# Performance work log

Hardware: AMD Instinct MI355X
Metric: run time of the kernel (lower is better)

The kernel has to match this reference:

```python
import jax, jax.numpy as jnp
import numpy as np
from jax.scipy.special import erf, erfc

N_ATOMS = 4096
BOX_L = 60.0
CUTOFF = 9.0
GRID = (64, 64, 64)
ORDER = 4
ALPHA = 0.34
COULOMB = 138.935456


def _bspline_weights(t, order):
    # Cardinal B-spline recursion (OpenMM/NNPOps convention).
    # w[..., j] = M_order(t + order - 1 - j), t in [0, 1)
    w = jnp.zeros(t.shape + (order,), t.dtype)
    w = w.at[..., 0].set(1.0 - t)
    w = w.at[..., 1].set(t)
    for k in range(3, order + 1):
        div = 1.0 / (k - 1)
        new = jnp.zeros_like(w)
        new = new.at[..., k - 1].set(div * t * w[..., k - 2])
        for j in range(1, k - 1):
            new = new.at[..., k - 1 - j].set(
                div * ((t + j) * w[..., k - 2 - j] + (k - j - t) * w[..., k - 1 - j]))
        new = new.at[..., 0].set(div * (1.0 - t) * w[..., 0])
        w = new
    return w


def _bspline_moduli(K, order):
    # |b(m)|^2 = 1 / |sum_k M_n(k+1) exp(2 pi i m k / K)|^2
    w = _bspline_weights(jnp.zeros((), jnp.float32), order)  # w[j] = M_n(n-1-j)
    mvals = w[::-1][1:]                                      # M_n(1), ..., M_n(n-1)
    data = jnp.zeros((K,), jnp.float32).at[jnp.arange(order - 1)].set(mvals)
    d2 = jnp.abs(jnp.fft.fft(data)) ** 2
    return 1.0 / jnp.maximum(d2, 1e-7)


def _min_image(delta, box, inv_box):
    s = delta @ inv_box
    s = s - jnp.round(s)
    return s @ box


def _pme_energy(positions, charges, box_vectors, exclusions):
    N = positions.shape[0]
    Kx, Ky, Kz = GRID
    inv_box = jnp.linalg.inv(box_vectors)

    # ---------------- direct space: erfc-screened pairwise sum with cutoff & exclusions
    delta = positions[:, None, :] - positions[None, :, :]          # [N,N,3]
    delta = _min_image(delta, box_vectors, inv_box)
    r2 = jnp.sum(delta * delta, axis=-1)                           # [N,N]
    rows = jnp.broadcast_to(jnp.arange(N)[:, None], exclusions.shape)
    excl_cols = jnp.where(exclusions >= 0, exclusions, rows)       # map padding -1 -> self
    excl_mask = jnp.zeros((N, N), bool).at[rows, excl_cols].set(True)
    pair_mask = jnp.triu(jnp.ones((N, N), bool), 1) & (r2 < CUTOFF ** 2) & (~excl_mask)
    r = jnp.sqrt(jnp.where(pair_mask, r2, 1.0))
    qq = charges[:, None] * charges[None, :]
    edir = COULOMB * jnp.sum(jnp.where(pair_mask, qq * erfc(ALPHA * r) / r, 0.0))

    # ---------------- reciprocal space: B-spline spread -> FFT -> influence function
    frac = positions @ inv_box
    frac = frac - jnp.floor(frac)                                  # wrap into [0,1)
    u = frac * jnp.asarray(GRID, frac.dtype)                       # [N,3] grid coords
    base = jnp.floor(u).astype(jnp.int32)
    t = u - jnp.floor(u)
    wx = _bspline_weights(t[:, 0], ORDER)                          # [N,order]
    wy = _bspline_weights(t[:, 1], ORDER)
    wz = _bspline_weights(t[:, 2], ORDER)
    offs = jnp.arange(ORDER, dtype=jnp.int32) - (ORDER - 1)        # weight j -> floor(u)-n+1+j
    ix = (base[:, 0:1] + offs) % Kx
    iy = (base[:, 1:2] + offs) % Ky
    iz = (base[:, 2:3] + offs) % Kz
    vals = (charges[:, None, None, None] * wx[:, :, None, None]
            * wy[:, None, :, None] * wz[:, None, None, :])         # [N,n,n,n]
    flat = (ix[:, :, None, None] * Ky + iy[:, None, :, None]) * Kz + iz[:, None, None, :]
    grid = jnp.zeros(Kx * Ky * Kz, positions.dtype).at[flat.reshape(-1)].add(
        vals.reshape(-1)).reshape(GRID)

    Fq = jnp.fft.fftn(grid)
    mx = (jnp.fft.fftfreq(Kx) * Kx).astype(positions.dtype)
    my = (jnp.fft.fftfreq(Ky) * Ky).astype(positions.dtype)
    mz = (jnp.fft.fftfreq(Kz) * Kz).astype(positions.dtype)
    m = jnp.stack(jnp.meshgrid(mx, my, mz, indexing='ij'), axis=-1)  # [Kx,Ky,Kz,3]
    kvec = m @ inv_box.T                                             # reciprocal vectors
    msq = jnp.sum(kvec * kvec, axis=-1)
    nonzero = msq > 0
    influence = jnp.where(nonzero,
                          jnp.exp(-(jnp.pi ** 2) * msq / ALPHA ** 2)
                          / jnp.where(nonzero, msq, 1.0), 0.0)
    bmod = (_bspline_moduli(Kx, ORDER)[:, None, None]
            * _bspline_moduli(Ky, ORDER)[None, :, None]
            * _bspline_moduli(Kz, ORDER)[None, None, :])
    V = jnp.abs(jnp.linalg.det(box_vectors))
    sq = Fq.real ** 2 + Fq.imag ** 2
    erec = COULOMB / (2.0 * jnp.pi * V) * jnp.sum(influence * bmod * sq)

    # self-energy correction
    eself = -COULOMB * ALPHA / jnp.sqrt(jnp.pi) * jnp.sum(charges ** 2)

    # exclusion correction: remove reciprocal contribution of excluded pairs
    de = positions[:, None, :] - positions[excl_cols]              # [N,E,3]
    de = _min_image(de, box_vectors, inv_box)
    re2 = jnp.sum(de * de, axis=-1)
    valid = (exclusions >= 0) & (re2 > 0)
    re = jnp.sqrt(jnp.where(valid, re2, 1.0))
    qe = charges[:, None] * charges[excl_cols]
    eexcl = -0.5 * COULOMB * jnp.sum(jnp.where(valid, qe * erf(ALPHA * re) / re, 0.0))

    return edir + erec + eself + eexcl


def setup_inputs():
    key = jax.random.key(0)
    k1, k2 = jax.random.split(key)
    positions = jax.random.uniform(k1, (N_ATOMS, 3), jnp.float32) * BOX_L
    charges = jax.random.normal(k2, (N_ATOMS,), jnp.float32) * 0.5
    charges = charges - jnp.mean(charges)  # neutral system
    box_vectors = jnp.eye(3, dtype=jnp.float32) * BOX_L
    idx = jnp.arange(N_ATOMS, dtype=jnp.int32)
    exclusions = jnp.stack([(idx - 1) % N_ATOMS, (idx + 1) % N_ATOMS], axis=1)  # symmetric chain
    return {"positions": positions, "charges": charges,
            "box_vectors": box_vectors, "exclusions": exclusions}


def reference(positions, charges, box_vectors, exclusions):
    return _pme_energy(positions, charges, box_vectors, exclusions)
```

## Files before the change

### kernel.cpp

```cpp
#include <hip/hip_runtime.h>
#include <math.h>
#include <stdint.h>

#define KG 64
#define KG3 (KG * KG * KG)
#define MZK 33
#define ALPHA 0.34f
#define COULOMB 138.935456f
#define CUTOFF2 81.0f
#define PI_F 3.14159265358979323846f

struct BoxInfo {
    float inv[9];
    float vol;
    bool diag;
};
__device__ __forceinline__ BoxInfo load_box(const float* __restrict__ box) {
    BoxInfo b;
    float b0 = box[0], b1 = box[1], b2 = box[2];
    float b3 = box[3], b4 = box[4], b5 = box[5];
    float b6 = box[6], b7 = box[7], b8 = box[8];
    float det = b0 * (b4 * b8 - b5 * b7) - b1 * (b3 * b8 - b5 * b6) + b2 * (b3 * b7 - b4 * b6);
    float id = 1.0f / det;
    b.inv[0] = (b4 * b8 - b5 * b7) * id;
    b.inv[1] = (b2 * b7 - b1 * b8) * id;
    b.inv[2] = (b1 * b5 - b2 * b4) * id;
    b.inv[3] = (b5 * b6 - b3 * b8) * id;
    b.inv[4] = (b0 * b8 - b2 * b6) * id;
    b.inv[5] = (b2 * b3 - b0 * b5) * id;
    b.inv[6] = (b3 * b7 - b4 * b6) * id;
    b.inv[7] = (b1 * b6 - b0 * b7) * id;
    b.inv[8] = (b0 * b4 - b1 * b3) * id;
    b.vol = fabsf(det);
    b.diag = (b1 == 0.0f) && (b2 == 0.0f) && (b3 == 0.0f) && (b5 == 0.0f) && (b6 == 0.0f) &&
             (b7 == 0.0f);
    return b;
}

__device__ __forceinline__ float erfc_fast(float x) {
    float t = __builtin_amdgcn_rcpf(fmaf(0.3275911f, x, 1.0f));
    float p = fmaf(t, 1.061405429f, -1.453152027f);
    p = fmaf(t, p, 1.421413741f);
    p = fmaf(t, p, -0.284496736f);
    p = fmaf(t, p, 0.254829592f);
    return t * p * __expf(-x * x);
}

__device__ __forceinline__ void bspline4(float t, float* w) {
    float w0 = 1.0f - t, w1 = t;
    float a2 = 0.5f * t * w1;
    float a1 = 0.5f * ((t + 1.0f) * w0 + (2.0f - t) * w1);
    float a0 = 0.5f * (1.0f - t) * w0;
    const float d = 1.0f / 3.0f;
    w[3] = d * t * a2;
    w[2] = d * ((t + 1.0f) * a1 + (3.0f - t) * a2);
    w[1] = d * ((t + 2.0f) * a0 + (2.0f - t) * a1);
    w[0] = d * (1.0f - t) * a0;
}

__global__ __launch_bounds__(256) void spread_kernel(const float* __restrict__ pos,
                                                     const float* __restrict__ chg,
                                                     const float* __restrict__ box,
                                                     float* __restrict__ grid,
                                                     float4* __restrict__ pxq, int N) {
    int t4 = blockIdx.x * blockDim.x + threadIdx.x;
    int i = t4 >> 2, jx = t4 & 3;
    if (i >= N) return;
    BoxInfo B = load_box(box);
    float p0 = pos[3 * i], p1 = pos[3 * i + 1], p2 = pos[3 * i + 2];
    float q = chg[i];
    if (jx == 0) pxq[i] = make_float4(p0, p1, p2, q);
    float w[3][4];
    int idx[3][4];
#pragma unroll
    for (int a = 0; a < 3; a++) {
        float f = p0 * B.inv[0 * 3 + a] + p1 * B.inv[1 * 3 + a] + p2 * B.inv[2 * 3 + a];
        f -= floorf(f);
        float u = f * (float)KG;
        float fu = floorf(u);
        int base = (int)fu;
        float tt = u - fu;
        bspline4(tt, w[a]);
#pragma unroll
        for (int j = 0; j < 4; j++) idx[a][j] = (base - 3 + j + 2 * KG) & (KG - 1);
    }
    float qx = q * w[0][jx];
    int bx = idx[0][jx] * KG;
#pragma unroll
    for (int jy = 0; jy < 4; jy++) {
        float qxy = qx * w[1][jy];
        int bxy = (bx + idx[1][jy]) * KG;
#pragma unroll
        for (int jz = 0; jz < 4; jz++) {
            atomicAdd(&grid[bxy + idx[2][jz]], qxy * w[2][jz]);
        }
    }
}

#define DIB 256
#define DJT 32
__global__ __launch_bounds__(256) void direct_kernel(const float4* __restrict__ pxq,
                                                     const float* __restrict__ box,
                                                     const int* __restrict__ excl, int N, int E,
                                                     double* __restrict__ partD) {
    int ib = blockIdx.x * DIB, jb = blockIdx.y * DJT;
    if (jb + DJT <= ib) return;

    __shared__ float4 sj[DJT];
    __shared__ double wsum[4];
    int tid = threadIdx.x;
    if (tid < DJT) {
        int jg0 = jb + tid;
        sj[tid] = (jg0 < N) ? pxq[jg0] : make_float4(0.0f, 0.0f, 0.0f, 0.0f);
    }
    __syncthreads();

    BoxInfo B = load_box(box);
    double e = 0.0;
    int i = ib + tid;
    if (i < N) {
        float4 me = pxq[i];
        float xi = me.x, yi = me.y, zi = me.z, qi = me.w;
        int ex0 = -1, ex1 = -1;
        int ne = (E < 8) ? E : 8;
        int ex[8];
        for (int k = 0; k < ne; k++) ex[k] = excl[i * E + k];

        float fsum = 0.0f;
        if (B.diag) {
            float Lx = box[0], Ly = box[4], Lz = box[8];
            float ivx = B.inv[0], ivy = B.inv[4], ivz = B.inv[8];
#pragma unroll 8
            for (int jj = 0; jj < DJT; jj++) {
                float4 o = sj[jj];
                int jg = jb + jj;
                float dx = xi - o.x, dy = yi - o.y, dz = zi - o.z;
                dx -= rintf(dx * ivx) * Lx;
                dy -= rintf(dy * ivy) * Ly;
                dz -= rintf(dz * ivz) * Lz;
                float r2 = fmaf(dx, dx, fmaf(dy, dy, dz * dz));
                bool valid = (r2 < CUTOFF2) & (jg > i) & (jg < N);
                for (int k = 0; k < ne; k++) valid = valid & (ex[k] != jg);
                float r2m = valid ? r2 : 1.0f;
                float rinv = __builtin_amdgcn_rsqf(r2m);
                float r = r2m * rinv;
                float g = erfc_fast(ALPHA * r) * rinv;
                float qqm = valid ? qi * o.w : 0.0f;
                fsum = fmaf(qqm, g, fsum);
            }
        } else {
#pragma unroll 4
            for (int jj = 0; jj < DJT; jj++) {
                float4 o = sj[jj];
                int jg = jb + jj;
                float dx = xi - o.x, dy = yi - o.y, dz = zi - o.z;
                float s0 = dx * B.inv[0] + dy * B.inv[3] + dz * B.inv[6];
                float s1 = dx * B.inv[1] + dy * B.inv[4] + dz * B.inv[7];
                float s2 = dx * B.inv[2] + dy * B.inv[5] + dz * B.inv[8];
                s0 -= rintf(s0);
                s1 -= rintf(s1);
                s2 -= rintf(s2);
                float ddx = s0 * box[0] + s1 * box[3] + s2 * box[6];
                float ddy = s0 * box[1] + s1 * box[4] + s2 * box[7];
                float ddz = s0 * box[2] + s1 * box[5] + s2 * box[8];
                float r2 = fmaf(ddx, ddx, fmaf(ddy, ddy, ddz * ddz));
                bool valid = (r2 < CUTOFF2) & (jg > i) & (jg < N);
                for (int k = 0; k < ne; k++) valid = valid & (ex[k] != jg);
                float r2m = valid ? r2 : 1.0f;
                float rinv = __builtin_amdgcn_rsqf(r2m);
                float r = r2m * rinv;
                float g = erfc_fast(ALPHA * r) * rinv;
                float qqm = valid ? qi * o.w : 0.0f;
                fsum = fmaf(qqm, g, fsum);
            }
        }
        e = (double)(COULOMB * fsum);

        if (jb == ib) {
            const float inv_sqrt_pi = 0.5641895835477563f;
            float corr = -ALPHA * inv_sqrt_pi * qi * qi;
            for (int k = 0; k < ne; k++) {
                int j = ex[k];
                if (j < 0) continue;
                float4 o = pxq[j];
                float dx = xi - o.x, dy = yi - o.y, dz = zi - o.z;
                if (B.diag) {
                    dx -= rintf(dx * B.inv[0]) * box[0];
                    dy -= rintf(dy * B.inv[4]) * box[4];
                    dz -= rintf(dz * B.inv[8]) * box[8];
                } else {
                    float s0 = dx * B.inv[0] + dy * B.inv[3] + dz * B.inv[6];
                    float s1 = dx * B.inv[1] + dy * B.inv[4] + dz * B.inv[7];
                    float s2 = dx * B.inv[2] + dy * B.inv[5] + dz * B.inv[8];
                    s0 -= rintf(s0);
                    s1 -= rintf(s1);
                    s2 -= rintf(s2);
                    dx = s0 * box[0] + s1 * box[3] + s2 * box[6];
                    dy = s0 * box[1] + s1 * box[4] + s2 * box[7];
                    dz = s0 * box[2] + s1 * box[5] + s2 * box[8];
                }
                float r2 = dx * dx + dy * dy + dz * dz;
                if (r2 > 0.0f) {
                    float rinv = __builtin_amdgcn_rsqf(r2);
                    float r = r2 * rinv;
                    float erfv = 1.0f - erfc_fast(ALPHA * r);
                    corr += -0.5f * qi * o.w * erfv * rinv;
                }
            }
            e += (double)(COULOMB * corr);
        }
    }
#pragma unroll
    for (int off = 32; off > 0; off >>= 1) e += __shfl_down(e, off, 64);
    if ((tid & 63) == 0) wsum[tid >> 6] = e;
    __syncthreads();
    if (tid == 0)
        partD[blockIdx.y * gridDim.x + blockIdx.x] = wsum[0] + wsum[1] + wsum[2] + wsum[3];
}

struct Tw8 {
    float wc[8], ws[8], c8, s8, c1, s1;
};
__device__ __forceinline__ Tw8 make_tw8(int m) {
    Tw8 T;
    float s1, c1;
    __sincosf(-2.0f * PI_F * (float)m / (float)KG, &s1, &c1);
    T.c1 = c1;
    T.s1 = s1;
    float c2 = c1 * c1 - s1 * s1, s2 = 2.0f * c1 * s1;
    float c4 = c2 * c2 - s2 * s2, s4 = 2.0f * c2 * s2;
    T.c8 = c4 * c4 - s4 * s4;
    T.s8 = 2.0f * c4 * s4;
    T.wc[0] = 1.0f;
    T.ws[0] = 0.0f;
    T.wc[1] = c1;
    T.ws[1] = s1;
    T.wc[2] = c2;
    T.ws[2] = s2;
    T.wc[3] = c2 * c1 - s2 * s1;
    T.ws[3] = c2 * s1 + s2 * c1;
    T.wc[4] = c4;
    T.ws[4] = s4;
    T.wc[5] = c4 * c1 - s4 * s1;
    T.ws[5] = c4 * s1 + s4 * c1;
    T.wc[6] = c4 * c2 - s4 * s2;
    T.ws[6] = c4 * s2 + s4 * c2;
    T.wc[7] = c4 * T.wc[3] - s4 * T.ws[3];
    T.ws[7] = c4 * T.ws[3] + s4 * T.wc[3];
    return T;
}

__global__ __launch_bounds__(256) void dft_z(const float* __restrict__ grid,
                                             float2* __restrict__ bufA) {
    __shared__ float g[4][KG];
    int tid = threadIdx.x, wv = tid >> 6, ln = tid & 63;
    int line = blockIdx.x * 4 + wv;
    g[wv][ln] = grid[line * KG + ln];
    __syncthreads();
    Tw8 T = make_tw8(ln);
    float rr[8] = {0}, ii[8] = {0};
#pragma unroll
    for (int s = 0; s < 8; s++) {
#pragma unroll
        for (int gg = 0; gg < 8; gg++) {
            float gv = g[wv][s * 8 + gg];
            rr[gg] = fmaf(gv, T.wc[gg], rr[gg]);
            ii[gg] = fmaf(gv, T.ws[gg], ii[gg]);
            float nc = T.wc[gg] * T.c8 - T.ws[gg] * T.s8;
            T.ws[gg] = T.wc[gg] * T.s8 + T.ws[gg] * T.c8;
            T.wc[gg] = nc;
        }
    }
    if (ln < MZK) {
        float re = ((rr[0] + rr[1]) + (rr[2] + rr[3])) + ((rr[4] + rr[5]) + (rr[6] + rr[7]));
        float im = ((ii[0] + ii[1]) + (ii[2] + ii[3])) + ((ii[4] + ii[5]) + (ii[6] + ii[7]));
        int ix = line >> 6, iy = line & 63;
        bufA[(ix * KG + ln) * KG + iy] = make_float2(re, im);
    }
}

__global__ __launch_bounds__(256) void dft_y(const float2* __restrict__ bufA,
                                             float2* __restrict__ bufB) {
    __shared__ float2 c[4][KG];
    int tid = threadIdx.x, wv = tid >> 6, ln = tid & 63;
    int idx = blockIdx.x * 4 + wv;
    if (idx >= KG * MZK) return;
    int ix = idx / MZK, mz = idx - ix * MZK;
    c[wv][ln] = bufA[(ix * KG + mz) * KG + ln];
    __syncthreads();
    Tw8 T = make_tw8(ln);
    float rr[8] = {0}, ii[8] = {0};
#pragma unroll
    for (int s = 0; s < 8; s++) {
#pragma unroll
        for (int gg = 0; gg < 8; gg++) {
            float2 a = c[wv][s * 8 + gg];
            rr[gg] += a.x * T.wc[gg] - a.y * T.ws[gg];
            ii[gg] += a.x * T.ws[gg] + a.y * T.wc[gg];
            float nc = T.wc[gg] * T.c8 - T.ws[gg] * T.s8;
            T.ws[gg] = T.wc[gg] * T.s8 + T.ws[gg] * T.c8;
            T.wc[gg] = nc;
        }
    }
    float re = ((rr[0] + rr[1]) + (rr[2] + rr[3])) + ((rr[4] + rr[5]) + (rr[6] + rr[7]));
    float im = ((ii[0] + ii[1]) + (ii[2] + ii[3])) + ((ii[4] + ii[5]) + (ii[6] + ii[7]));
    bufB[(ln * MZK + mz) * KG + ix] = make_float2(re, im);
}

__device__ __forceinline__ float bmod4(float c1, float s1) {
    float c2 = 2.0f * c1 * c1 - 1.0f;
    float s2 = 2.0f * s1 * c1;
    float br = (1.0f + 4.0f * c1 + c2) * (1.0f / 6.0f);
    float bi = (4.0f * s1 + s2) * (1.0f / 6.0f);
    float d2 = br * br + bi * bi;
    return 1.0f / fmaxf(d2, 1e-7f);
}

__global__ __launch_bounds__(256) void dft_x_reduce(const float2* __restrict__ bufB,
                                                    const float* __restrict__ box,
                                                    double* __restrict__ partR) {
    __shared__ float2 c[4][KG];
    int tid = threadIdx.x, wv = tid >> 6, ln = tid & 63;
    int idx = blockIdx.x * 4 + wv;
    if (idx >= KG * MZK) return;
    int my = idx / MZK, mz = idx - my * MZK;
    c[wv][ln] = bufB[(my * MZK + mz) * KG + ln];
    __syncthreads();
    Tw8 T = make_tw8(ln);
    float rr[8] = {0}, ii[8] = {0};
#pragma unroll
    for (int s = 0; s < 8; s++) {
#pragma unroll
        for (int gg = 0; gg < 8; gg++) {
            float2 a = c[wv][s * 8 + gg];
            rr[gg] += a.x * T.wc[gg] - a.y * T.ws[gg];
            ii[gg] += a.x * T.ws[gg] + a.y * T.wc[gg];
            float nc = T.wc[gg] * T.c8 - T.ws[gg] * T.s8;
            T.ws[gg] = T.wc[gg] * T.s8 + T.ws[gg] * T.c8;
            T.wc[gg] = nc;
        }
    }
    float re = ((rr[0] + rr[1]) + (rr[2] + rr[3])) + ((rr[4] + rr[5]) + (rr[6] + rr[7]));
    float im = ((ii[0] + ii[1]) + (ii[2] + ii[3])) + ((ii[4] + ii[5]) + (ii[6] + ii[7]));
    float sq = re * re + im * im;

    BoxInfo B = load_box(box);
    int mx = ln;
    int msx = (mx < KG / 2) ? mx : mx - KG;
    int msy = (my < KG / 2) ? my : my - KG;
    int msz = (mz < KG / 2) ? mz : mz - KG;
    float fmx = (float)msx, fmy = (float)msy, fmz = (float)msz;
    float kx = fmx * B.inv[0] + fmy * B.inv[1] + fmz * B.inv[2];
    float ky = fmx * B.inv[3] + fmy * B.inv[4] + fmz * B.inv[5];
    float kz = fmx * B.inv[6] + fmy * B.inv[7] + fmz * B.inv[8];
    float msq = kx * kx + ky * ky + kz * kz;
    const float cexp = (PI_F * PI_F) / (ALPHA * ALPHA);
    float infl = (msq > 0.0f) ? __expf(-cexp * msq) / msq : 0.0f;

    float bx_ = bmod4(T.c1, T.s1);
    float sy, cy, sz, cz;
    __sincosf(2.0f * PI_F * (float)my / (float)KG, &sy, &cy);
    __sincosf(2.0f * PI_F * (float)mz / (float)KG, &sz, &cz);
    float by_ = bmod4(cy, sy);
    float bz_ = bmod4(cz, sz);

    float wgt = (mz == 0 || mz == 32) ? 1.0f : 2.0f;
    float pref = COULOMB / (2.0f * PI_F * B.vol);
    double term = (double)(wgt * pref * infl * bx_ * by_ * bz_ * sq);

#pragma unroll
    for (int off = 32; off > 0; off >>= 1) term += __shfl_down(term, off, 64);
    if (ln == 0) partR[idx] = term;
}

__global__ __launch_bounds__(1024) void final_reduce(const double* __restrict__ parts, int n,
                                                     float* __restrict__ out) {
    __shared__ double wsum[16];
    int tid = threadIdx.x;
    double s = 0.0;
    for (int k = tid; k < n; k += 1024) s += parts[k];
#pragma unroll
    for (int off = 32; off > 0; off >>= 1) s += __shfl_down(s, off, 64);
    if ((tid & 63) == 0) wsum[tid >> 6] = s;
    __syncthreads();
    if (tid == 0) {
        double t = 0.0;
#pragma unroll
        for (int w = 0; w < 16; w++) t += wsum[w];
        out[0] = (float)t;
    }
}


extern "C" void kernel_launch(void* const* d_in, const int* in_sizes, int n_in,
                              void* d_out, int out_size, void* d_ws, size_t ws_size,
                              hipStream_t stream) {
    const float* pos = (const float*)d_in[0];
    const float* chg = (const float*)d_in[1];
    const float* box = (const float*)d_in[2];
    const int* excl = (const int*)d_in[3];
    int N = in_sizes[0] / 3;
    int E = in_sizes[3] / N;

    char* ws = (char*)d_ws;
    double* partD = (double*)(ws + 4096);
    double* partR = (double*)(ws + 20480);
    double* parts = (double*)(ws + 4096);
    float* grid = (float*)(ws + 65536);
    float2* bufA = (float2*)(ws + 65536 + 4 * (size_t)KG3);
    float2* bufB = (float2*)(ws + 65536 + 12 * (size_t)KG3);
    float4* pxq = (float4*)bufB;

    hipMemsetAsync(ws, 0, 65536 + 4 * (size_t)KG3, stream);

    spread_kernel<<<(4 * N + 255) / 256, 256, 0, stream>>>(pos, chg, box, grid, pxq, N);

    int nib = (N + DIB - 1) / DIB;
    int njt = (N + DJT - 1) / DJT;
    dim3 dg(nib, njt);
    direct_kernel<<<dg, 256, 0, stream>>>(pxq, box, excl, N, E, partD);

    dft_z<<<KG * KG / 4, 256, 0, stream>>>(grid, bufA);
    int nlines = KG * MZK;
    dft_y<<<(nlines + 3) / 4, 256, 0, stream>>>(bufA, bufB);
    dft_x_reduce<<<(nlines + 3) / 4, 256, 0, stream>>>(bufB, box, partR);

    int nparts = nib * njt + nlines;
    final_reduce<<<1, 1024, 0, stream>>>(parts, nparts, (float*)d_out);
}
```

Before: 132.5 us.

## Fuse spread with direct sum, merge z/y DFTs, fold final reduce into x-DFT

Charge spreading and the direct-space pair sum now run as different block ranges of one launch. The z and y DFT passes are merged into one 512-thread kernel per x-plane that keeps the intermediate in shared memory. The final reduction moves into the x-DFT kernel through a last-block atomic counter. Together these drop the launch count from six to three and remove the bufA round trip through global memory. The cost is that the y pass runs on only 64 blocks, giving low parallelism, and every direct block now reads positions from the strided pos and chg arrays instead of packed float4s.

```diff
diff --git a/kernel.cpp b/kernel.cpp
--- a/kernel.cpp
+++ b/kernel.cpp
@@ -9,6 +9,8 @@
 #define COULOMB 138.935456f
 #define CUTOFF2 81.0f
 #define PI_F 3.14159265358979323846f
+#define DIB 256
+#define DJT 32
 
 struct BoxInfo {
     float inv[9];
@@ -56,166 +58,6 @@
     w[2] = d * ((t + 1.0f) * a1 + (3.0f - t) * a2);
     w[1] = d * ((t + 2.0f) * a0 + (2.0f - t) * a1);
     w[0] = d * (1.0f - t) * a0;
-}
-
-__global__ __launch_bounds__(256) void spread_kernel(const float* __restrict__ pos,
-                                                     const float* __restrict__ chg,
-                                                     const float* __restrict__ box,
-                                                     float* __restrict__ grid,
-                                                     float4* __restrict__ pxq, int N) {
-    int t4 = blockIdx.x * blockDim.x + threadIdx.x;
-    int i = t4 >> 2, jx = t4 & 3;
-    if (i >= N) return;
-    BoxInfo B = load_box(box);
-    float p0 = pos[3 * i], p1 = pos[3 * i + 1], p2 = pos[3 * i + 2];
-    float q = chg[i];
-    if (jx == 0) pxq[i] = make_float4(p0, p1, p2, q);
-    float w[3][4];
-    int idx[3][4];
-#pragma unroll
-    for (int a = 0; a < 3; a++) {
-        float f = p0 * B.inv[0 * 3 + a] + p1 * B.inv[1 * 3 + a] + p2 * B.inv[2 * 3 + a];
-        f -= floorf(f);
-        float u = f * (float)KG;
-        float fu = floorf(u);
-        int base = (int)fu;
-        float tt = u - fu;
-        bspline4(tt, w[a]);
-#pragma unroll
-        for (int j = 0; j < 4; j++) idx[a][j] = (base - 3 + j + 2 * KG) & (KG - 1);
-    }
-    float qx = q * w[0][jx];
-    int bx = idx[0][jx] * KG;
-#pragma unroll
-    for (int jy = 0; jy < 4; jy++) {
-        float qxy = qx * w[1][jy];
-        int bxy = (bx + idx[1][jy]) * KG;
-#pragma unroll
-        for (int jz = 0; jz < 4; jz++) {
-            atomicAdd(&grid[bxy + idx[2][jz]], qxy * w[2][jz]);
-        }
-    }
-}
-
-#define DIB 256
-#define DJT 32
-__global__ __launch_bounds__(256) void direct_kernel(const float4* __restrict__ pxq,
-                                                     const float* __restrict__ box,
-                                                     const int* __restrict__ excl, int N, int E,
-                                                     double* __restrict__ partD) {
-    int ib = blockIdx.x * DIB, jb = blockIdx.y * DJT;
-    if (jb + DJT <= ib) return;
-
-    __shared__ float4 sj[DJT];
-    __shared__ double wsum[4];
-    int tid = threadIdx.x;
-    if (tid < DJT) {
-        int jg0 = jb + tid;
-        sj[tid] = (jg0 < N) ? pxq[jg0] : make_float4(0.0f, 0.0f, 0.0f, 0.0f);
-    }
-    __syncthreads();
-
-    BoxInfo B = load_box(box);
-    double e = 0.0;
-    int i = ib + tid;
-    if (i < N) {
-        float4 me = pxq[i];
-        float xi = me.x, yi = me.y, zi = me.z, qi = me.w;
-        int ex0 = -1, ex1 = -1;
-        int ne = (E < 8) ? E : 8;
-        int ex[8];
-        for (int k = 0; k < ne; k++) ex[k] = excl[i * E + k];
-
-        float fsum = 0.0f;
-        if (B.diag) {
-            float Lx = box[0], Ly = box[4], Lz = box[8];
-            float ivx = B.inv[0], ivy = B.inv[4], ivz = B.inv[8];
-#pragma unroll 8
-            for (int jj = 0; jj < DJT; jj++) {
-                float4 o = sj[jj];
-                int jg = jb + jj;
-                float dx = xi - o.x, dy = yi - o.y, dz = zi - o.z;
-                dx -= rintf(dx * ivx) * Lx;
-                dy -= rintf(dy * ivy) * Ly;
-                dz -= rintf(dz * ivz) * Lz;
-                float r2 = fmaf(dx, dx, fmaf(dy, dy, dz * dz));
-                bool valid = (r2 < CUTOFF2) & (jg > i) & (jg < N);
-                for (int k = 0; k < ne; k++) valid = valid & (ex[k] != jg);
-                float r2m = valid ? r2 : 1.0f;
-                float rinv = __builtin_amdgcn_rsqf(r2m);
-                float r = r2m * rinv;
-                float g = erfc_fast(ALPHA * r) * rinv;
-                float qqm = valid ? qi * o.w : 0.0f;
-                fsum = fmaf(qqm, g, fsum);
-            }
-        } else {
-#pragma unroll 4
-            for (int jj = 0; jj < DJT; jj++) {
-                float4 o = sj[jj];
-                int jg = jb + jj;
-                float dx = xi - o.x, dy = yi - o.y, dz = zi - o.z;
-                float s0 = dx * B.inv[0] + dy * B.inv[3] + dz * B.inv[6];
-                float s1 = dx * B.inv[1] + dy * B.inv[4] + dz * B.inv[7];
-                float s2 = dx * B.inv[2] + dy * B.inv[5] + dz * B.inv[8];
-                s0 -= rintf(s0);
-                s1 -= rintf(s1);
-                s2 -= rintf(s2);
-                float ddx = s0 * box[0] + s1 * box[3] + s2 * box[6];
-                float ddy = s0 * box[1] + s1 * box[4] + s2 * box[7];
-                float ddz = s0 * box[2] + s1 * box[5] + s2 * box[8];
-                float r2 = fmaf(ddx, ddx, fmaf(ddy, ddy, ddz * ddz));
-                bool valid = (r2 < CUTOFF2) & (jg > i) & (jg < N);
-                for (int k = 0; k < ne; k++) valid = valid & (ex[k] != jg);
-                float r2m = valid ? r2 : 1.0f;
-                float rinv = __builtin_amdgcn_rsqf(r2m);
-                float r = r2m * rinv;
-                float g = erfc_fast(ALPHA * r) * rinv;
-                float qqm = valid ? qi * o.w : 0.0f;
-                fsum = fmaf(qqm, g, fsum);
-            }
-        }
-        e = (double)(COULOMB * fsum);
-
-        if (jb == ib) {
-            const float inv_sqrt_pi = 0.5641895835477563f;
-            float corr = -ALPHA * inv_sqrt_pi * qi * qi;
-            for (int k = 0; k < ne; k++) {
-                int j = ex[k];
-                if (j < 0) continue;
-                float4 o = pxq[j];
-                float dx = xi - o.x, dy = yi - o.y, dz = zi - o.z;
-                if (B.diag) {
-                    dx -= rintf(dx * B.inv[0]) * box[0];
-                    dy -= rintf(dy * B.inv[4]) * box[4];
-                    dz -= rintf(dz * B.inv[8]) * box[8];
-                } else {
-                    float s0 = dx * B.inv[0] + dy * B.inv[3] + dz * B.inv[6];
-                    float s1 = dx * B.inv[1] + dy * B.inv[4] + dz * B.inv[7];
-                    float s2 = dx * B.inv[2] + dy * B.inv[5] + dz * B.inv[8];
-                    s0 -= rintf(s0);
-                    s1 -= rintf(s1);
-                    s2 -= rintf(s2);
-                    dx = s0 * box[0] + s1 * box[3] + s2 * box[6];
-                    dy = s0 * box[1] + s1 * box[4] + s2 * box[7];
-                    dz = s0 * box[2] + s1 * box[5] + s2 * box[8];
-                }
-                float r2 = dx * dx + dy * dy + dz * dz;
-                if (r2 > 0.0f) {
-                    float rinv = __builtin_amdgcn_rsqf(r2);
-                    float r = r2 * rinv;
-                    float erfv = 1.0f - erfc_fast(ALPHA * r);
-                    corr += -0.5f * qi * o.w * erfv * rinv;
-                }
-            }
-            e += (double)(COULOMB * corr);
-        }
-    }
-#pragma unroll
-    for (int off = 32; off > 0; off >>= 1) e += __shfl_down(e, off, 64);
-    if ((tid & 63) == 0) wsum[tid >> 6] = e;
-    __syncthreads();
-    if (tid == 0)
-        partD[blockIdx.y * gridDim.x + blockIdx.x] = wsum[0] + wsum[1] + wsum[2] + wsum[3];
 }
 
 struct Tw8 {
@@ -250,63 +92,6 @@
     return T;
 }
 
-__global__ __launch_bounds__(256) void dft_z(const float* __restrict__ grid,
-                                             float2* __restrict__ bufA) {
-    __shared__ float g[4][KG];
-    int tid = threadIdx.x, wv = tid >> 6, ln = tid & 63;
-    int line = blockIdx.x * 4 + wv;
-    g[wv][ln] = grid[line * KG + ln];
-    __syncthreads();
-    Tw8 T = make_tw8(ln);
-    float rr[8] = {0}, ii[8] = {0};
-#pragma unroll
-    for (int s = 0; s < 8; s++) {
-#pragma unroll
-        for (int gg = 0; gg < 8; gg++) {
-            float gv = g[wv][s * 8 + gg];
-            rr[gg] = fmaf(gv, T.wc[gg], rr[gg]);
-            ii[gg] = fmaf(gv, T.ws[gg], ii[gg]);
-            float nc = T.wc[gg] * T.c8 - T.ws[gg] * T.s8;
-            T.ws[gg] = T.wc[gg] * T.s8 + T.ws[gg] * T.c8;
-            T.wc[gg] = nc;
-        }
-    }
-    if (ln < MZK) {
-        float re = ((rr[0] + rr[1]) + (rr[2] + rr[3])) + ((rr[4] + rr[5]) + (rr[6] + rr[7]));
-        float im = ((ii[0] + ii[1]) + (ii[2] + ii[3])) + ((ii[4] + ii[5]) + (ii[6] + ii[7]));
-        int ix = line >> 6, iy = line & 63;
-        bufA[(ix * KG + ln) * KG + iy] = make_float2(re, im);
-    }
-}
-
-__global__ __launch_bounds__(256) void dft_y(const float2* __restrict__ bufA,
-                                             float2* __restrict__ bufB) {
-    __shared__ float2 c[4][KG];
-    int tid = threadIdx.x, wv = tid >> 6, ln = tid & 63;
-    int idx = blockIdx.x * 4 + wv;
-    if (idx >= KG * MZK) return;
-    int ix = idx / MZK, mz = idx - ix * MZK;
-    c[wv][ln] = bufA[(ix * KG + mz) * KG + ln];
-    __syncthreads();
-    Tw8 T = make_tw8(ln);
-    float rr[8] = {0}, ii[8] = {0};
-#pragma unroll
-    for (int s = 0; s < 8; s++) {
-#pragma unroll
-        for (int gg = 0; gg < 8; gg++) {
-            float2 a = c[wv][s * 8 + gg];
-            rr[gg] += a.x * T.wc[gg] - a.y * T.ws[gg];
-            ii[gg] += a.x * T.ws[gg] + a.y * T.wc[gg];
-            float nc = T.wc[gg] * T.c8 - T.ws[gg] * T.s8;
-            T.ws[gg] = T.wc[gg] * T.s8 + T.ws[gg] * T.c8;
-            T.wc[gg] = nc;
-        }
-    }
-    float re = ((rr[0] + rr[1]) + (rr[2] + rr[3])) + ((rr[4] + rr[5]) + (rr[6] + rr[7]));
-    float im = ((ii[0] + ii[1]) + (ii[2] + ii[3])) + ((ii[4] + ii[5]) + (ii[6] + ii[7]));
-    bufB[(ln * MZK + mz) * KG + ix] = make_float2(re, im);
-}
-
 __device__ __forceinline__ float bmod4(float c1, float s1) {
     float c2 = 2.0f * c1 * c1 - 1.0f;
     float s2 = 2.0f * s1 * c1;
@@ -316,28 +101,272 @@
     return 1.0f / fmaxf(d2, 1e-7f);
 }
 
-__global__ __launch_bounds__(256) void dft_x_reduce(const float2* __restrict__ bufB,
-                                                    const float* __restrict__ box,
-                                                    double* __restrict__ partR) {
+__global__ __launch_bounds__(256) void spread_direct(const float* __restrict__ pos,
+                                                     const float* __restrict__ chg,
+                                                     const float* __restrict__ box,
+                                                     const int* __restrict__ excl, int N, int E,
+                                                     float* __restrict__ grid,
+                                                     double* __restrict__ partD) {
+    int tid = threadIdx.x;
+    const int nib = (N + DIB - 1) / DIB;
+    const int njt = (N + DJT - 1) / DJT;
+    const int DU = nib * njt;
+    int u = blockIdx.x;
+
+    if (u >= DU) {
+        int t4 = (u - DU) * 256 + tid;
+        int i = t4 >> 2, jx = t4 & 3;
+        if (i >= N) return;
+        BoxInfo B = load_box(box);
+        float p0 = pos[3 * i], p1 = pos[3 * i + 1], p2 = pos[3 * i + 2];
+        float q = chg[i];
+        float w[3][4];
+        int idx[3][4];
+#pragma unroll
+        for (int a = 0; a < 3; a++) {
+            float f = p0 * B.inv[0 * 3 + a] + p1 * B.inv[1 * 3 + a] + p2 * B.inv[2 * 3 + a];
+            f -= floorf(f);
+            float uu = f * (float)KG;
+            float fu = floorf(uu);
+            int base = (int)fu;
+            float tt = uu - fu;
+            bspline4(tt, w[a]);
+#pragma unroll
+            for (int j = 0; j < 4; j++) idx[a][j] = (base - 3 + j + 2 * KG) & (KG - 1);
+        }
+        float qx = q * w[0][jx];
+        int bx = idx[0][jx] * KG;
+#pragma unroll
+        for (int jy = 0; jy < 4; jy++) {
+            float qxy = qx * w[1][jy];
+            int bxy = (bx + idx[1][jy]) * KG;
+#pragma unroll
+            for (int jz = 0; jz < 4; jz++) {
+                atomicAdd(&grid[bxy + idx[2][jz]], qxy * w[2][jz]);
+            }
+        }
+        return;
+    }
+
+    int du = u;
+    int ib = (du % nib) * DIB, jb = (du / nib) * DJT;
+    if (jb + DJT <= ib) {
+        if (tid == 0) partD[du] = 0.0;
+        return;
+    }
+
+    __shared__ float4 sj[DJT];
+    __shared__ double wsum[4];
+    if (tid < DJT) {
+        int jg0 = jb + tid;
+        sj[tid] = (jg0 < N) ? make_float4(pos[3 * jg0], pos[3 * jg0 + 1], pos[3 * jg0 + 2],
+                                          chg[jg0])
+                            : make_float4(0.0f, 0.0f, 0.0f, 0.0f);
+    }
+    __syncthreads();
+
+    BoxInfo B = load_box(box);
+    double e = 0.0;
+    int i = ib + tid;
+    if (i < N) {
+        float xi = pos[3 * i], yi = pos[3 * i + 1], zi = pos[3 * i + 2], qi = chg[i];
+        int ne = (E < 8) ? E : 8;
+        int ex[8];
+        for (int k = 0; k < ne; k++) ex[k] = excl[i * E + k];
+
+        float fsum = 0.0f;
+        if (B.diag) {
+            float Lx = box[0], Ly = box[4], Lz = box[8];
+            float ivx = B.inv[0], ivy = B.inv[4], ivz = B.inv[8];
+#pragma unroll 8
+            for (int jj = 0; jj < DJT; jj++) {
+                float4 o = sj[jj];
+                int jg = jb + jj;
+                float dx = xi - o.x, dy = yi - o.y, dz = zi - o.z;
+                dx -= rintf(dx * ivx) * Lx;
+                dy -= rintf(dy * ivy) * Ly;
+                dz -= rintf(dz * ivz) * Lz;
+                float r2 = fmaf(dx, dx, fmaf(dy, dy, dz * dz));
+                bool valid = (r2 < CUTOFF2) & (jg > i) & (jg < N);
+                for (int k = 0; k < ne; k++) valid = valid & (ex[k] != jg);
+                float r2m = valid ? r2 : 1.0f;
+                float rinv = __builtin_amdgcn_rsqf(r2m);
+                float r = r2m * rinv;
+                float g = erfc_fast(ALPHA * r) * rinv;
+                float qqm = valid ? qi * o.w : 0.0f;
+                fsum = fmaf(qqm, g, fsum);
+            }
+        } else {
+#pragma unroll 4
+            for (int jj = 0; jj < DJT; jj++) {
+                float4 o = sj[jj];
+                int jg = jb + jj;
+                float dx = xi - o.x, dy = yi - o.y, dz = zi - o.z;
+                float s0 = dx * B.inv[0] + dy * B.inv[3] + dz * B.inv[6];
+                float s1 = dx * B.inv[1] + dy * B.inv[4] + dz * B.inv[7];
+                float s2 = dx * B.inv[2] + dy * B.inv[5] + dz * B.inv[8];
+                s0 -= rintf(s0);
+                s1 -= rintf(s1);
+                s2 -= rintf(s2);
+                float ddx = s0 * box[0] + s1 * box[3] + s2 * box[6];
+                float ddy = s0 * box[1] + s1 * box[4] + s2 * box[7];
+                float ddz = s0 * box[2] + s1 * box[5] + s2 * box[8];
+                float r2 = fmaf(ddx, ddx, fmaf(ddy, ddy, ddz * ddz));
+                bool valid = (r2 < CUTOFF2) & (jg > i) & (jg < N);
+                for (int k = 0; k < ne; k++) valid = valid & (ex[k] != jg);
+                float r2m = valid ? r2 : 1.0f;
+                float rinv = __builtin_amdgcn_rsqf(r2m);
+                float r = r2m * rinv;
+                float g = erfc_fast(ALPHA * r) * rinv;
+                float qqm = valid ? qi * o.w : 0.0f;
+                fsum = fmaf(qqm, g, fsum);
+            }
+        }
+        e = (double)(COULOMB * fsum);
+
+        if (jb == ib) {
+            const float inv_sqrt_pi = 0.5641895835477563f;
+            float corr = -ALPHA * inv_sqrt_pi * qi * qi;
+            for (int k = 0; k < ne; k++) {
+                int j = ex[k];
+                if (j < 0) continue;
+                float ox = pos[3 * j], oy = pos[3 * j + 1], oz = pos[3 * j + 2];
+                float qj = chg[j];
+                float dx = xi - ox, dy = yi - oy, dz = zi - oz;
+                if (B.diag) {
+                    dx -= rintf(dx * B.inv[0]) * box[0];
+                    dy -= rintf(dy * B.inv[4]) * box[4];
+                    dz -= rintf(dz * B.inv[8]) * box[8];
+                } else {
+                    float s0 = dx * B.inv[0] + dy * B.inv[3] + dz * B.inv[6];
+                    float s1 = dx * B.inv[1] + dy * B.inv[4] + dz * B.inv[7];
+                    float s2 = dx * B.inv[2] + dy * B.inv[5] + dz * B.inv[8];
+                    s0 -= rintf(s0);
+                    s1 -= rintf(s1);
+                    s2 -= rintf(s2);
+                    dx = s0 * box[0] + s1 * box[3] + s2 * box[6];
+                    dy = s0 * box[1] + s1 * box[4] + s2 * box[7];
+                    dz = s0 * box[2] + s1 * box[5] + s2 * box[8];
+                }
+                float r2 = dx * dx + dy * dy + dz * dz;
+                if (r2 > 0.0f) {
+                    float rinv = __builtin_amdgcn_rsqf(r2);
+                    float r = r2 * rinv;
+                    float erfv = 1.0f - erfc_fast(ALPHA * r);
+                    corr += -0.5f * qi * qj * erfv * rinv;
+                }
+            }
+            e += (double)(COULOMB * corr);
+        }
+    }
+#pragma unroll
+    for (int off = 32; off > 0; off >>= 1) e += __shfl_down(e, off, 64);
+    if ((tid & 63) == 0) wsum[tid >> 6] = e;
+    __syncthreads();
+    if (tid == 0) partD[du] = wsum[0] + wsum[1] + wsum[2] + wsum[3];
+}
+
+__global__ __launch_bounds__(512) void dft_zy(const float* __restrict__ grid,
+                                              float2* __restrict__ bufB) {
+    __shared__ float gin[KG * KG];
+    __shared__ float zre[KG * MZK];
+    __shared__ float zim[KG * MZK];
+    int tid = threadIdx.x, wv = tid >> 6, ln = tid & 63;
+    int ix = blockIdx.x;
+
+    const float4* g4 = reinterpret_cast<const float4*>(grid + ix * (KG * KG));
+    float4* s4 = reinterpret_cast<float4*>(gin);
+#pragma unroll
+    for (int k = 0; k < 2; k++) s4[k * 512 + tid] = g4[k * 512 + tid];
+    __syncthreads();
+
+    Tw8 T0 = make_tw8(ln);
+
+#pragma unroll
+    for (int it = 0; it < 8; it++) {
+        int iy = wv * 8 + it;
+        float wc[8], ws_[8];
+#pragma unroll
+        for (int g = 0; g < 8; g++) {
+            wc[g] = T0.wc[g];
+            ws_[g] = T0.ws[g];
+        }
+        float rr[8] = {0, 0, 0, 0, 0, 0, 0, 0}, ii[8] = {0, 0, 0, 0, 0, 0, 0, 0};
+#pragma unroll
+        for (int s = 0; s < 8; s++) {
+#pragma unroll
+            for (int g = 0; g < 8; g++) {
+                float gv = gin[iy * KG + s * 8 + g];
+                rr[g] = fmaf(gv, wc[g], rr[g]);
+                ii[g] = fmaf(gv, ws_[g], ii[g]);
+                float nc = wc[g] * T0.c8 - ws_[g] * T0.s8;
+                ws_[g] = wc[g] * T0.s8 + ws_[g] * T0.c8;
+                wc[g] = nc;
+            }
+        }
+        if (ln < MZK) {
+            float re = ((rr[0] + rr[1]) + (rr[2] + rr[3])) + ((rr[4] + rr[5]) + (rr[6] + rr[7]));
+            float im = ((ii[0] + ii[1]) + (ii[2] + ii[3])) + ((ii[4] + ii[5]) + (ii[6] + ii[7]));
+            zre[iy * MZK + ln] = re;
+            zim[iy * MZK + ln] = im;
+        }
+    }
+    __syncthreads();
+
+    for (int mz = wv; mz < MZK; mz += 8) {
+        float wc[8], ws_[8];
+#pragma unroll
+        for (int g = 0; g < 8; g++) {
+            wc[g] = T0.wc[g];
+            ws_[g] = T0.ws[g];
+        }
+        float rr[8] = {0, 0, 0, 0, 0, 0, 0, 0}, ii[8] = {0, 0, 0, 0, 0, 0, 0, 0};
+#pragma unroll
+        for (int s = 0; s < 8; s++) {
+#pragma unroll
+            for (int g = 0; g < 8; g++) {
+                int iy = s * 8 + g;
+                float ar = zre[iy * MZK + mz];
+                float ai = zim[iy * MZK + mz];
+                rr[g] += ar * wc[g] - ai * ws_[g];
+                ii[g] += ar * ws_[g] + ai * wc[g];
+                float nc = wc[g] * T0.c8 - ws_[g] * T0.s8;
+                ws_[g] = wc[g] * T0.s8 + ws_[g] * T0.c8;
+                wc[g] = nc;
+            }
+        }
+        float re = ((rr[0] + rr[1]) + (rr[2] + rr[3])) + ((rr[4] + rr[5]) + (rr[6] + rr[7]));
+        float im = ((ii[0] + ii[1]) + (ii[2] + ii[3])) + ((ii[4] + ii[5]) + (ii[6] + ii[7]));
+        bufB[(ln * MZK + mz) * KG + ix] = make_float2(re, im);
+    }
+}
+
+__global__ __launch_bounds__(256) void dft_x_final(const float2* __restrict__ bufB,
+                                                   const float* __restrict__ box,
+                                                   double* __restrict__ partR,
+                                                   const double* __restrict__ parts, int np,
+                                                   unsigned* __restrict__ cnt,
+                                                   float* __restrict__ out) {
     __shared__ float2 c[4][KG];
+    __shared__ double fw[4];
+    __shared__ unsigned lastFlag;
     int tid = threadIdx.x, wv = tid >> 6, ln = tid & 63;
     int idx = blockIdx.x * 4 + wv;
-    if (idx >= KG * MZK) return;
     int my = idx / MZK, mz = idx - my * MZK;
     c[wv][ln] = bufB[(my * MZK + mz) * KG + ln];
     __syncthreads();
     Tw8 T = make_tw8(ln);
-    float rr[8] = {0}, ii[8] = {0};
+    float rr[8] = {0, 0, 0, 0, 0, 0, 0, 0}, ii[8] = {0, 0, 0, 0, 0, 0, 0, 0};
 #pragma unroll
     for (int s = 0; s < 8; s++) {
 #pragma unroll
-        for (int gg = 0; gg < 8; gg++) {
-            float2 a = c[wv][s * 8 + gg];
-            rr[gg] += a.x * T.wc[gg] - a.y * T.ws[gg];
-            ii[gg] += a.x * T.ws[gg] + a.y * T.wc[gg];
-            float nc = T.wc[gg] * T.c8 - T.ws[gg] * T.s8;
-            T.ws[gg] = T.wc[gg] * T.s8 + T.ws[gg] * T.c8;
-            T.wc[gg] = nc;
+        for (int g = 0; g < 8; g++) {
+            float2 a = c[wv][s * 8 + g];
+            rr[g] += a.x * T.wc[g] - a.y * T.ws[g];
+            ii[g] += a.x * T.ws[g] + a.y * T.wc[g];
+            float nc = T.wc[g] * T.c8 - T.ws[g] * T.s8;
+            T.ws[g] = T.wc[g] * T.s8 + T.ws[g] * T.c8;
+            T.wc[g] = nc;
         }
     }
     float re = ((rr[0] + rr[1]) + (rr[2] + rr[3])) + ((rr[4] + rr[5]) + (rr[6] + rr[7]));
@@ -371,23 +400,24 @@
 #pragma unroll
     for (int off = 32; off > 0; off >>= 1) term += __shfl_down(term, off, 64);
     if (ln == 0) partR[idx] = term;
-}
-
-__global__ __launch_bounds__(1024) void final_reduce(const double* __restrict__ parts, int n,
-                                                     float* __restrict__ out) {
-    __shared__ double wsum[16];
-    int tid = threadIdx.x;
-    double s = 0.0;
-    for (int k = tid; k < n; k += 1024) s += parts[k];
-#pragma unroll
-    for (int off = 32; off > 0; off >>= 1) s += __shfl_down(s, off, 64);
-    if ((tid & 63) == 0) wsum[tid >> 6] = s;
+
     __syncthreads();
     if (tid == 0) {
-        double t = 0.0;
-#pragma unroll
-        for (int w = 0; w < 16; w++) t += wsum[w];
-        out[0] = (float)t;
+        __threadfence();
+        unsigned old = atomicAdd(cnt, 1u);
+        lastFlag = (old == gridDim.x - 1) ? 1u : 0u;
+    }
+    __syncthreads();
+    if (lastFlag) {
+        if (tid == 0) __threadfence();
+        __syncthreads();
+        double s = 0.0;
+        for (int k = tid; k < np; k += 256) s += parts[k];
+#pragma unroll
+        for (int off = 32; off > 0; off >>= 1) s += __shfl_down(s, off, 64);
+        if ((tid & 63) == 0) fw[tid >> 6] = s;
+        __syncthreads();
+        if (tid == 0) out[0] = (float)(fw[0] + fw[1] + fw[2] + fw[3]);
     }
 }
 
@@ -403,28 +433,25 @@
     int E = in_sizes[3] / N;
 
     char* ws = (char*)d_ws;
+    unsigned* cnt = (unsigned*)ws;
     double* partD = (double*)(ws + 4096);
     double* partR = (double*)(ws + 20480);
-    double* parts = (double*)(ws + 4096);
     float* grid = (float*)(ws + 65536);
-    float2* bufA = (float2*)(ws + 65536 + 4 * (size_t)KG3);
-    float2* bufB = (float2*)(ws + 65536 + 12 * (size_t)KG3);
-    float4* pxq = (float4*)bufB;
+    float2* bufB = (float2*)(ws + 65536 + 4 * (size_t)KG3);
+    float* outp = (float*)d_out;
+
+    const int nib = (N + DIB - 1) / DIB;
+    const int njt = (N + DJT - 1) / DJT;
+    const int DU = nib * njt;
+    const int SB = (4 * N + 255) / 256;
+    const int nlines = KG * MZK;
+    const int np = DU + nlines;
 
     hipMemsetAsync(ws, 0, 65536 + 4 * (size_t)KG3, stream);
 
-    spread_kernel<<<(4 * N + 255) / 256, 256, 0, stream>>>(pos, chg, box, grid, pxq, N);
-
-    int nib = (N + DIB - 1) / DIB;
-    int njt = (N + DJT - 1) / DJT;
-    dim3 dg(nib, njt);
-    direct_kernel<<<dg, 256, 0, stream>>>(pxq, box, excl, N, E, partD);
-
-    dft_z<<<KG * KG / 4, 256, 0, stream>>>(grid, bufA);
-    int nlines = KG * MZK;
-    dft_y<<<(nlines + 3) / 4, 256, 0, stream>>>(bufA, bufB);
-    dft_x_reduce<<<(nlines + 3) / 4, 256, 0, stream>>>(bufB, box, partR);
-
-    int nparts = nib * njt + nlines;
-    final_reduce<<<1, 1024, 0, stream>>>(parts, nparts, (float*)d_out);
-}
+    spread_direct<<<DU + SB, 256, 0, stream>>>(pos, chg, box, excl, N, E, grid, partD);
+
+    dft_zy<<<KG, 512, 0, stream>>>(grid, bufB);
+
+    dft_x_final<<<nlines / 4, 256, 0, stream>>>(bufB, box, partR, partD, np, cnt, outp);
+}
```

Measured after the change: 210.5 us. +58.9%, slower.

## Fuse spread with direct sum and fold final reduction into last DFT kernel

Applied to the files above, without the earlier changes.

Merges the charge-spreading and direct-space kernels into one launch, with block ranges partitioned between the two tasks. The direct part now reads positions and charges straight from the inputs instead of a packed float4 buffer. The final reduction moves into the x-DFT kernel using an atomic counter that picks the last block to finish. Two kernel launches and their serial dependencies go away, at the cost of strided uncoalesced position loads, a fence plus atomic per block, and a serialized tail reduction in the last block.

```diff
diff --git a/kernel.cpp b/kernel.cpp
--- a/kernel.cpp
+++ b/kernel.cpp
@@ -9,6 +9,8 @@
 #define COULOMB 138.935456f
 #define CUTOFF2 81.0f
 #define PI_F 3.14159265358979323846f
+#define DIB 256
+#define DJT 32
 
 struct BoxInfo {
     float inv[9];
@@ -58,60 +60,108 @@
     w[0] = d * (1.0f - t) * a0;
 }
 
-__global__ __launch_bounds__(256) void spread_kernel(const float* __restrict__ pos,
+struct Tw8 {
+    float wc[8], ws[8], c8, s8, c1, s1;
+};
+__device__ __forceinline__ Tw8 make_tw8(int m) {
+    Tw8 T;
+    float s1, c1;
+    __sincosf(-2.0f * PI_F * (float)m / (float)KG, &s1, &c1);
+    T.c1 = c1;
+    T.s1 = s1;
+    float c2 = c1 * c1 - s1 * s1, s2 = 2.0f * c1 * s1;
+    float c4 = c2 * c2 - s2 * s2, s4 = 2.0f * c2 * s2;
+    T.c8 = c4 * c4 - s4 * s4;
+    T.s8 = 2.0f * c4 * s4;
+    T.wc[0] = 1.0f;
+    T.ws[0] = 0.0f;
+    T.wc[1] = c1;
+    T.ws[1] = s1;
+    T.wc[2] = c2;
+    T.ws[2] = s2;
+    T.wc[3] = c2 * c1 - s2 * s1;
+    T.ws[3] = c2 * s1 + s2 * c1;
+    T.wc[4] = c4;
+    T.ws[4] = s4;
+    T.wc[5] = c4 * c1 - s4 * s1;
+    T.ws[5] = c4 * s1 + s4 * c1;
+    T.wc[6] = c4 * c2 - s4 * s2;
+    T.ws[6] = c4 * s2 + s4 * c2;
+    T.wc[7] = c4 * T.wc[3] - s4 * T.ws[3];
+    T.ws[7] = c4 * T.ws[3] + s4 * T.wc[3];
+    return T;
+}
+
+__device__ __forceinline__ float bmod4(float c1, float s1) {
+    float c2 = 2.0f * c1 * c1 - 1.0f;
+    float s2 = 2.0f * s1 * c1;
+    float br = (1.0f + 4.0f * c1 + c2) * (1.0f / 6.0f);
+    float bi = (4.0f * s1 + s2) * (1.0f / 6.0f);
+    float d2 = br * br + bi * bi;
+    return 1.0f / fmaxf(d2, 1e-7f);
+}
+
+__global__ __launch_bounds__(256) void spread_direct(const float* __restrict__ pos,
                                                      const float* __restrict__ chg,
                                                      const float* __restrict__ box,
+                                                     const int* __restrict__ excl, int N, int E,
                                                      float* __restrict__ grid,
-                                                     float4* __restrict__ pxq, int N) {
-    int t4 = blockIdx.x * blockDim.x + threadIdx.x;
-    int i = t4 >> 2, jx = t4 & 3;
-    if (i >= N) return;
-    BoxInfo B = load_box(box);
-    float p0 = pos[3 * i], p1 = pos[3 * i + 1], p2 = pos[3 * i + 2];
-    float q = chg[i];
-    if (jx == 0) pxq[i] = make_float4(p0, p1, p2, q);
-    float w[3][4];
-    int idx[3][4];
-#pragma unroll
-    for (int a = 0; a < 3; a++) {
-        float f = p0 * B.inv[0 * 3 + a] + p1 * B.inv[1 * 3 + a] + p2 * B.inv[2 * 3 + a];
-        f -= floorf(f);
-        float u = f * (float)KG;
-        float fu = floorf(u);
-        int base = (int)fu;
-        float tt = u - fu;
-        bspline4(tt, w[a]);
-#pragma unroll
-        for (int j = 0; j < 4; j++) idx[a][j] = (base - 3 + j + 2 * KG) & (KG - 1);
-    }
-    float qx = q * w[0][jx];
-    int bx = idx[0][jx] * KG;
-#pragma unroll
-    for (int jy = 0; jy < 4; jy++) {
-        float qxy = qx * w[1][jy];
-        int bxy = (bx + idx[1][jy]) * KG;
-#pragma unroll
-        for (int jz = 0; jz < 4; jz++) {
-            atomicAdd(&grid[bxy + idx[2][jz]], qxy * w[2][jz]);
-        }
-    }
-}
-
-#define DIB 256
-#define DJT 32
-__global__ __launch_bounds__(256) void direct_kernel(const float4* __restrict__ pxq,
-                                                     const float* __restrict__ box,
-                                                     const int* __restrict__ excl, int N, int E,
                                                      double* __restrict__ partD) {
-    int ib = blockIdx.x * DIB, jb = blockIdx.y * DJT;
-    if (jb + DJT <= ib) return;
+    int tid = threadIdx.x;
+    const int nib = (N + DIB - 1) / DIB;
+    const int njt = (N + DJT - 1) / DJT;
+    const int DU = nib * njt;
+    int u = blockIdx.x;
+
+    if (u >= DU) {
+        int t4 = (u - DU) * 256 + tid;
+        int i = t4 >> 2, jx = t4 & 3;
+        if (i >= N) return;
+        BoxInfo B = load_box(box);
+        float p0 = pos[3 * i], p1 = pos[3 * i + 1], p2 = pos[3 * i + 2];
+        float q = chg[i];
+        float w[3][4];
+        int idx[3][4];
+#pragma unroll
+        for (int a = 0; a < 3; a++) {
+            float f = p0 * B.inv[0 * 3 + a] + p1 * B.inv[1 * 3 + a] + p2 * B.inv[2 * 3 + a];
+            f -= floorf(f);
+            float uu = f * (float)KG;
+            float fu = floorf(uu);
+            int base = (int)fu;
+            float tt = uu - fu;
+            bspline4(tt, w[a]);
+#pragma unroll
+            for (int j = 0; j < 4; j++) idx[a][j] = (base - 3 + j + 2 * KG) & (KG - 1);
+        }
+        float qx = q * w[0][jx];
+        int bx = idx[0][jx] * KG;
+#pragma unroll
+        for (int jy = 0; jy < 4; jy++) {
+            float qxy = qx * w[1][jy];
+            int bxy = (bx + idx[1][jy]) * KG;
+#pragma unroll
+            for (int jz = 0; jz < 4; jz++) {
+                atomicAdd(&grid[bxy + idx[2][jz]], qxy * w[2][jz]);
+            }
+        }
+        return;
+    }
+
+    int du = u;
+    int ib = (du % nib) * DIB, jb = (du / nib) * DJT;
+    if (jb + DJT <= ib) {
+        if (tid == 0) partD[du] = 0.0;
+        return;
+    }
 
     __shared__ float4 sj[DJT];
     __shared__ double wsum[4];
-    int tid = threadIdx.x;
     if (tid < DJT) {
         int jg0 = jb + tid;
-        sj[tid] = (jg0 < N) ? pxq[jg0] : make_float4(0.0f, 0.0f, 0.0f, 0.0f);
+        sj[tid] = (jg0 < N) ? make_float4(pos[3 * jg0], pos[3 * jg0 + 1], pos[3 * jg0 + 2],
+                                          chg[jg0])
+                            : make_float4(0.0f, 0.0f, 0.0f, 0.0f);
     }
     __syncthreads();
 
@@ -119,9 +169,7 @@
     double e = 0.0;
     int i = ib + tid;
     if (i < N) {
-        float4 me = pxq[i];
-        float xi = me.x, yi = me.y, zi = me.z, qi = me.w;
-        int ex0 = -1, ex1 = -1;
+        float xi = pos[3 * i], yi = pos[3 * i + 1], zi = pos[3 * i + 2], qi = chg[i];
         int ne = (E < 8) ? E : 8;
         int ex[8];
         for (int k = 0; k < ne; k++) ex[k] = excl[i * E + k];
@@ -182,8 +230,9 @@
             for (int k = 0; k < ne; k++) {
                 int j = ex[k];
                 if (j < 0) continue;
-                float4 o = pxq[j];
-                float dx = xi - o.x, dy = yi - o.y, dz = zi - o.z;
+                float ox = pos[3 * j], oy = pos[3 * j + 1], oz = pos[3 * j + 2];
+                float qj = chg[j];
+                float dx = xi - ox, dy = yi - oy, dz = zi - oz;
                 if (B.diag) {
                     dx -= rintf(dx * B.inv[0]) * box[0];
                     dy -= rintf(dy * B.inv[4]) * box[4];
@@ -204,7 +253,7 @@
                     float rinv = __builtin_amdgcn_rsqf(r2);
                     float r = r2 * rinv;
                     float erfv = 1.0f - erfc_fast(ALPHA * r);
-                    corr += -0.5f * qi * o.w * erfv * rinv;
+                    corr += -0.5f * qi * qj * erfv * rinv;
                 }
             }
             e += (double)(COULOMB * corr);
@@ -214,40 +263,7 @@
     for (int off = 32; off > 0; off >>= 1) e += __shfl_down(e, off, 64);
     if ((tid & 63) == 0) wsum[tid >> 6] = e;
     __syncthreads();
-    if (tid == 0)
-        partD[blockIdx.y * gridDim.x + blockIdx.x] = wsum[0] + wsum[1] + wsum[2] + wsum[3];
-}
-
-struct Tw8 {
-    float wc[8], ws[8], c8, s8, c1, s1;
-};
-__device__ __forceinline__ Tw8 make_tw8(int m) {
-    Tw8 T;
-    float s1, c1;
-    __sincosf(-2.0f * PI_F * (float)m / (float)KG, &s1, &c1);
-    T.c1 = c1;
-    T.s1 = s1;
-    float c2 = c1 * c1 - s1 * s1, s2 = 2.0f * c1 * s1;
-    float c4 = c2 * c2 - s2 * s2, s4 = 2.0f * c2 * s2;
-    T.c8 = c4 * c4 - s4 * s4;
-    T.s8 = 2.0f * c4 * s4;
-    T.wc[0] = 1.0f;
-    T.ws[0] = 0.0f;
-    T.wc[1] = c1;
-    T.ws[1] = s1;
-    T.wc[2] = c2;
-    T.ws[2] = s2;
-    T.wc[3] = c2 * c1 - s2 * s1;
-    T.ws[3] = c2 * s1 + s2 * c1;
-    T.wc[4] = c4;
-    T.ws[4] = s4;
-    T.wc[5] = c4 * c1 - s4 * s1;
-    T.ws[5] = c4 * s1 + s4 * c1;
-    T.wc[6] = c4 * c2 - s4 * s2;
-    T.ws[6] = c4 * s2 + s4 * c2;
-    T.wc[7] = c4 * T.wc[3] - s4 * T.ws[3];
-    T.ws[7] = c4 * T.ws[3] + s4 * T.wc[3];
-    return T;
+    if (tid == 0) partD[du] = wsum[0] + wsum[1] + wsum[2] + wsum[3];
 }
 
 __global__ __launch_bounds__(256) void dft_z(const float* __restrict__ grid,
@@ -307,22 +323,17 @@
     bufB[(ln * MZK + mz) * KG + ix] = make_float2(re, im);
 }
 
-__device__ __forceinline__ float bmod4(float c1, float s1) {
-    float c2 = 2.0f * c1 * c1 - 1.0f;
-    float s2 = 2.0f * s1 * c1;
-    float br = (1.0f + 4.0f * c1 + c2) * (1.0f / 6.0f);
-    float bi = (4.0f * s1 + s2) * (1.0f / 6.0f);
-    float d2 = br * br + bi * bi;
-    return 1.0f / fmaxf(d2, 1e-7f);
-}
-
-__global__ __launch_bounds__(256) void dft_x_reduce(const float2* __restrict__ bufB,
-                                                    const float* __restrict__ box,
-                                                    double* __restrict__ partR) {
+__global__ __launch_bounds__(256) void dft_x_final(const float2* __restrict__ bufB,
+                                                   const float* __restrict__ box,
+                                                   double* __restrict__ partR,
+                                                   const double* __restrict__ parts, int np,
+                                                   unsigned* __restrict__ cnt,
+                                                   float* __restrict__ out) {
     __shared__ float2 c[4][KG];
+    __shared__ double fw[4];
+    __shared__ unsigned lastFlag;
     int tid = threadIdx.x, wv = tid >> 6, ln = tid & 63;
     int idx = blockIdx.x * 4 + wv;
-    if (idx >= KG * MZK) return;
     int my = idx / MZK, mz = idx - my * MZK;
     c[wv][ln] = bufB[(my * MZK + mz) * KG + ln];
     __syncthreads();
@@ -371,23 +382,24 @@
 #pragma unroll
     for (int off = 32; off > 0; off >>= 1) term += __shfl_down(term, off, 64);
     if (ln == 0) partR[idx] = term;
-}
-
-__global__ __launch_bounds__(1024) void final_reduce(const double* __restrict__ parts, int n,
-                                                     float* __restrict__ out) {
-    __shared__ double wsum[16];
-    int tid = threadIdx.x;
-    double s = 0.0;
-    for (int k = tid; k < n; k += 1024) s += parts[k];
-#pragma unroll
-    for (int off = 32; off > 0; off >>= 1) s += __shfl_down(s, off, 64);
-    if ((tid & 63) == 0) wsum[tid >> 6] = s;
+
     __syncthreads();
     if (tid == 0) {
-        double t = 0.0;
-#pragma unroll
-        for (int w = 0; w < 16; w++) t += wsum[w];
-        out[0] = (float)t;
+        __threadfence();
+        unsigned old = atomicAdd(cnt, 1u);
+        lastFlag = (old == gridDim.x - 1) ? 1u : 0u;
+    }
+    __syncthreads();
+    if (lastFlag) {
+        if (tid == 0) __threadfence();
+        __syncthreads();
+        double s = 0.0;
+        for (int k = tid; k < np; k += 256) s += parts[k];
+#pragma unroll
+        for (int off = 32; off > 0; off >>= 1) s += __shfl_down(s, off, 64);
+        if ((tid & 63) == 0) fw[tid >> 6] = s;
+        __syncthreads();
+        if (tid == 0) out[0] = (float)(fw[0] + fw[1] + fw[2] + fw[3]);
     }
 }
 
@@ -403,28 +415,26 @@
     int E = in_sizes[3] / N;
 
     char* ws = (char*)d_ws;
+    unsigned* cnt = (unsigned*)ws;
     double* partD = (double*)(ws + 4096);
     double* partR = (double*)(ws + 20480);
-    double* parts = (double*)(ws + 4096);
     float* grid = (float*)(ws + 65536);
     float2* bufA = (float2*)(ws + 65536 + 4 * (size_t)KG3);
     float2* bufB = (float2*)(ws + 65536 + 12 * (size_t)KG3);
-    float4* pxq = (float4*)bufB;
+    float* outp = (float*)d_out;
+
+    const int nib = (N + DIB - 1) / DIB;
+    const int njt = (N + DJT - 1) / DJT;
+    const int DU = nib * njt;
+    const int SB = (4 * N + 255) / 256;
+    const int nlines = KG * MZK;
+    const int np = DU + nlines;
 
     hipMemsetAsync(ws, 0, 65536 + 4 * (size_t)KG3, stream);
 
-    spread_kernel<<<(4 * N + 255) / 256, 256, 0, stream>>>(pos, chg, box, grid, pxq, N);
-
-    int nib = (N + DIB - 1) / DIB;
-    int njt = (N + DJT - 1) / DJT;
-    dim3 dg(nib, njt);
-    direct_kernel<<<dg, 256, 0, stream>>>(pxq, box, excl, N, E, partD);
+    spread_direct<<<DU + SB, 256, 0, stream>>>(pos, chg, box, excl, N, E, grid, partD);
 
     dft_z<<<KG * KG / 4, 256, 0, stream>>>(grid, bufA);
-    int nlines = KG * MZK;
     dft_y<<<(nlines + 3) / 4, 256, 0, stream>>>(bufA, bufB);
-    dft_x_reduce<<<(nlines + 3) / 4, 256, 0, stream>>>(bufB, box, partR);
-
-    int nparts = nib * njt + nlines;
-    final_reduce<<<1, 1024, 0, stream>>>(parts, nparts, (float*)d_out);
-}
+    dft_x_final<<<(nlines + 3) / 4, 256, 0, stream>>>(bufB, box, partR, partD, np, cnt, outp);
+}
```

Measured after the change: 125.0 us. -5.7%, faster.
